# Kernel tuning notes

Measured on AMD Instinct MI355X. Metric: run time of the kernel, lower is better.

## Reference

```python
import jax, jax.numpy as jnp
import numpy as np

EMBED_DIM = 1024
NUM_HEADS = 16


def setup_inputs() -> dict:
    key = jax.random.key(0)
    k_x, k_w, k_b, k_ow, k_ob = jax.random.split(key, 5)
    B, S, E = 4, 2048, EMBED_DIM
    scale = 1.0 / np.sqrt(E)
    x = jax.random.normal(k_x, (B, S, E), dtype=jnp.float32)
    # nn.MultiheadAttention packed in-projection [3E, E] and out projection [E, E]
    in_proj_w = jax.random.uniform(k_w, (3 * E, E), dtype=jnp.float32, minval=-scale, maxval=scale)
    in_proj_b = jnp.zeros((3 * E,), dtype=jnp.float32)
    out_proj_w = jax.random.uniform(k_ow, (E, E), dtype=jnp.float32, minval=-scale, maxval=scale)
    out_proj_b = jnp.zeros((E,), dtype=jnp.float32)
    return {"x": x, "in_proj_w": in_proj_w, "in_proj_b": in_proj_b,
            "out_proj_w": out_proj_w, "out_proj_b": out_proj_b}


def reference(x, in_proj_w, in_proj_b, out_proj_w, out_proj_b):
    B, S, E = x.shape
    H = NUM_HEADS
    hd = E // H
    # packed QKV projection: [B,S,3E]
    qkv = x @ in_proj_w.T + in_proj_b
    q, k, v = jnp.split(qkv, 3, axis=-1)
    # [B,S,E] -> [B,H,S,hd]
    def to_heads(t):
        return t.reshape(B, S, H, hd).transpose(0, 2, 1, 3)
    q, k, v = to_heads(q), to_heads(k), to_heads(v)
    scale = 1.0 / jnp.sqrt(jnp.asarray(hd, dtype=x.dtype))
    scores = jnp.einsum('bhqd,bhkd->bhqk', q * scale, k)  # [B,H,S,S]
    # causal mask: position i attends to <= i (matches the -inf additive mask)
    causal = jnp.tril(jnp.ones((S, S), dtype=bool))
    scores = jnp.where(causal[None, None, :, :], scores, jnp.finfo(x.dtype).min)
    attn = jax.nn.softmax(scores, axis=-1)
    out = jnp.einsum('bhqk,bhkd->bhqd', attn, v)  # [B,H,S,hd]
    out = out.transpose(0, 2, 1, 3).reshape(B, S, E)
    return out @ out_proj_w.T + out_proj_b
```

## Files before the change

kernel.cpp:

```cpp
#include <hip/hip_runtime.h>
#include <stdint.h>

typedef _Float16 f16;
typedef _Float16 f16x2 __attribute__((ext_vector_type(2)));
typedef _Float16 f16x8 __attribute__((ext_vector_type(8)));
typedef float f32x4 __attribute__((ext_vector_type(4)));
typedef float f32x16 __attribute__((ext_vector_type(16)));
typedef uint32_t u32x4 __attribute__((ext_vector_type(4)));

#define B_   4
#define S_   2048
#define E_   1024
#define H_   16
#define HD_  64
#define BH_  (B_ * H_)

template <int N> struct IC { static constexpr int v = N; };

__device__ __forceinline__ void async_lds16(const void* g, void* l) {
    __builtin_amdgcn_global_load_lds(
        (__attribute__((address_space(1))) void*)(uintptr_t)g,
        (__attribute__((address_space(3))) void*)(uint32_t)(uintptr_t)l,
        16, 0, 0);
}

__global__ __launch_bounds__(256)
void cvt_f32_to_f16(const float* __restrict__ in, f16* __restrict__ out, int n8) {
    int i = blockIdx.x * 256 + threadIdx.x;
    if (i >= n8) return;
    const float4* p = (const float4*)in;
    float4 a = p[2 * i], b = p[2 * i + 1];
    f16x8 o;
    o[0] = (f16)a.x; o[1] = (f16)a.y; o[2] = (f16)a.z; o[3] = (f16)a.w;
    o[4] = (f16)b.x; o[5] = (f16)b.y; o[6] = (f16)b.z; o[7] = (f16)b.w;
    *(f16x8*)(out + 8 * (long)i) = o;
}

template <int MODE>
__global__ __launch_bounds__(256)
void gemm_bt(const f16* __restrict__ A, const f16* __restrict__ Bm,
             const float* __restrict__ bias, float* __restrict__ Cf,
             f16* __restrict__ qo, f16* __restrict__ ko, f16* __restrict__ vto,
             int M, int N, int K)
{
    __shared__ __align__(16) f16 As[2][128 * 32];
    __shared__ __align__(16) f16 Bs[2][128 * 32];
    const int tid = threadIdx.x;
    const int wave = tid >> 6, lane = tid & 63;
    const int lo = lane & 15, hi = lane >> 4;
    const int ntn = N >> 7;
    const int tm = blockIdx.x / ntn, tn = blockIdx.x % ntn;
    const long bm0 = (long)tm << 7, bn0 = (long)tn << 7;
    const int wr = (wave >> 1) << 6, wc = (wave & 1) << 6;

    int srow[2], sxc[2];
#pragma unroll
    for (int p = 0; p < 2; ++p) {
        const int c = p * 256 + tid;
        srow[p] = c >> 2;
        sxc[p]  = (((c & 3) ^ ((c >> 3) & 3))) * 8;
    }

#define GSTAGE(BUF, K0)  do {                                                     \
    _Pragma("unroll")                                                             \
    for (int p = 0; p < 2; ++p) {                                                 \
        const int base = (p * 256 + wave * 64) * 8;                               \
        async_lds16(A  + (bm0 + srow[p]) * K + (K0) + sxc[p], &As[BUF][base]);    \
        async_lds16(Bm + (bn0 + srow[p]) * K + (K0) + sxc[p], &Bs[BUF][base]);    \
    } } while (0)

    f32x4 acc[4][4] = {};

    auto compute = [&](auto bufc) {
        constexpr int BUF = decltype(bufc)::v;
        f16x8 af[4], bf[4];
#pragma unroll
        for (int mi = 0; mi < 4; ++mi) {
            const int row = wr + mi * 16 + lo;
            af[mi] = *(const f16x8*)&As[BUF][row * 32 + ((hi ^ ((row >> 1) & 3)) * 8)];
        }
#pragma unroll
        for (int ni = 0; ni < 4; ++ni) {
            const int row = wc + ni * 16 + lo;
            bf[ni] = *(const f16x8*)&Bs[BUF][row * 32 + ((hi ^ ((row >> 1) & 3)) * 8)];
        }
        __builtin_amdgcn_s_setprio(1);
#pragma unroll
        for (int mi = 0; mi < 4; ++mi)
#pragma unroll
            for (int ni = 0; ni < 4; ++ni)
                acc[mi][ni] = __builtin_amdgcn_mfma_f32_16x16x32_f16(
                    af[mi], bf[ni], acc[mi][ni], 0, 0, 0);
        __builtin_amdgcn_s_setprio(0);
    };

    GSTAGE(0, 0);
    __syncthreads();
    for (int k0 = 0; k0 < K; k0 += 64) {
        GSTAGE(1, k0 + 32);
        compute(IC<0>{});
        __syncthreads();
        if (k0 + 64 < K) GSTAGE(0, k0 + 64);
        compute(IC<1>{});
        __syncthreads();
    }
#undef GSTAGE

    if (MODE == 1) {
#pragma unroll
        for (int mi = 0; mi < 4; ++mi)
#pragma unroll
            for (int ni = 0; ni < 4; ++ni)
#pragma unroll
                for (int j = 0; j < 4; ++j) {
                    const long r  = bm0 + wr + mi * 16 + 4 * hi + j;
                    const int  cn = (int)bn0 + wc + ni * 16 + lo;
                    Cf[r * N + cn] = acc[mi][ni][j] + bias[cn];
                }
        return;
    }

    const int which = (int)(bn0 >> 10);
    if (which < 2) {
#pragma unroll
        for (int mi = 0; mi < 4; ++mi)
#pragma unroll
            for (int ni = 0; ni < 4; ++ni)
#pragma unroll
                for (int j = 0; j < 4; ++j) {
                    const long r  = bm0 + wr + mi * 16 + 4 * hi + j;
                    const int  cn = (int)bn0 + wc + ni * 16 + lo;
                    const int  e = cn & 1023, h = e >> 6, d = e & 63;
                    const int  b = (int)(r >> 11), s = (int)(r & 2047);
                    const long bh = (long)b * H_ + h;
                    const f16 hv = (f16)(acc[mi][ni][j] + bias[cn]);
                    if (which == 0) qo[(bh * S_ + s) * HD_ + d] = hv;
                    else            ko[(bh * S_ + s) * HD_ + d] = hv;
                }
    } else {
        f16* T = (wave < 2) ? ((f16*)As) + wave * 4096 : ((f16*)Bs) + (wave - 2) * 4096;
#pragma unroll
        for (int ni = 0; ni < 4; ++ni) {
            const int dl = ni * 16 + lo;
            const int dx = dl & 7;
#pragma unroll
            for (int mi = 0; mi < 4; ++mi)
#pragma unroll
                for (int j = 0; j < 4; ++j) {
                    const int sl = mi * 16 + 4 * hi + j;
                    const int cn = (int)bn0 + wc + ni * 16 + lo;
                    T[dl * 64 + ((((sl >> 3) ^ dx) << 3) | (sl & 7))] =
                        (f16)(acc[mi][ni][j] + bias[cn]);
                }
        }
        const int b = (int)(bm0 >> 11);
        const int sbase = (int)(bm0 & 2047) + wr;
        const int h = ((int)(bn0 & 1023) + wc) >> 6;
        const long vbase = (long)(b * H_ + h) * HD_;
#pragma unroll
        for (int it = 0; it < 8; ++it) {
            const int d = it * 8 + (lane >> 3);
            const int schunk = lane & 7;
            u32x4 val = *(const u32x4*)&T[d * 64 + ((schunk ^ (d & 7)) << 3)];
            *(u32x4*)&vto[(vbase + d) * S_ + sbase + schunk * 8] = val;
        }
    }
}

__global__ __launch_bounds__(256)
void attn_fwd(const f16* __restrict__ qb, const f16* __restrict__ kb,
              const f16* __restrict__ vtb, f16* __restrict__ ob)
{
    __shared__ __align__(16) f16 Ks[2][64 * 64];
    __shared__ __align__(16) f16 Vs[2][64 * 64];
    const int tid = threadIdx.x, wave = tid >> 6, lane = tid & 63;
    const int q32 = lane & 31, h2 = lane >> 5;
    const int bh = blockIdx.y;
    const int qtA = blockIdx.x;
    const int qtB = 15 - qtA;
    const int qwA = qtA * 128 + wave * 32;
    const int qwB = qtB * 128 + wave * 32;
    const long krow0 = (long)bh * S_;
    const long vrow0 = (long)bh * HD_;

#define STAGE(BUF, KV)  do {                                                      \
    _Pragma("unroll")                                                             \
    for (int p = 0; p < 2; ++p) {                                                 \
        const int n = p * 256 + tid;                                              \
        const int base = (p * 256 + wave * 64) * 8;                               \
        async_lds16(kb  + (krow0 + (KV) + (n & 63)) * HD_ + (n >> 6) * 8, &Ks[BUF][base]); \
        async_lds16(vtb + (vrow0 + (n & 63)) * S_ + (KV) + (n >> 6) * 8, &Vs[BUF][base]);  \
    } } while (0)

    f16x8 qfA[4], qfB[4];
    const f16 sch = (f16)0.1803368801f;
#pragma unroll
    for (int kkq = 0; kkq < 4; ++kkq) {
        qfA[kkq] = *(const f16x8*)&qb[(krow0 + qwA + q32) * HD_ + kkq * 16 + h2 * 8];
        qfB[kkq] = *(const f16x8*)&qb[(krow0 + qwB + q32) * HD_ + kkq * 16 + h2 * 8];
#pragma unroll
        for (int e = 0; e < 8; ++e) { qfA[kkq][e] *= sch; qfB[kkq][e] *= sch; }
    }

    f32x16 oaccA[2] = {}, oaccB[2] = {};
    float lA = 0.f, lB = 0.f;
    const f16x2 ones2 = { (f16)1.0f, (f16)1.0f };

    auto computeS = [&](auto bufc, auto spc, int t) {
        constexpr int BUF = decltype(bufc)::v;
        constexpr int SP  = decltype(spc)::v;
        const int qw = SP ? qwB : qwA;
        const f16x8* qf = SP ? qfB : qfA;
        f32x16* oacc = SP ? oaccB : oaccA;
        float& l_part = SP ? lB : lA;
        const int kv0 = t * 64;
        if (kv0 > qw + 31) return;
        const int qg = qw + q32;

        f32x16 sc[2] = {};
        __builtin_amdgcn_s_setprio(1);
#pragma unroll
        for (int kkq = 0; kkq < 4; ++kkq)
#pragma unroll
            for (int ni = 0; ni < 2; ++ni) {
                f16x8 kf = *(const f16x8*)&Ks[BUF][(((kkq * 2 + h2) * 64) + ni * 32 + q32) * 8];
                sc[ni] = __builtin_amdgcn_mfma_f32_32x32x16_f16(kf, qf[kkq], sc[ni], 0, 0, 0);
            }
        __builtin_amdgcn_s_setprio(0);

        const bool maskp = (kv0 + 63) > qw;
#pragma unroll
        for (int ni = 0; ni < 2; ++ni)
#pragma unroll
            for (int r = 0; r < 16; ++r) {
                float p = __builtin_amdgcn_exp2f(sc[ni][r]);
                const int kvg = kv0 + ni * 32 + (r & 3) + 8 * (r >> 2) + 4 * h2;
                if (maskp && kvg > qg) p = 0.0f;
                sc[ni][r] = p;
            }

        __builtin_amdgcn_s_setprio(1);
#pragma unroll
        for (int ni = 0; ni < 2; ++ni) {
            uint32_t u[8];
#pragma unroll
            for (int m = 0; m < 8; ++m) {
                auto hp = __builtin_amdgcn_cvt_pkrtz(sc[ni][2 * m], sc[ni][2 * m + 1]);
                u[m] = __builtin_bit_cast(uint32_t, hp);
                l_part = __builtin_amdgcn_fdot2(__builtin_bit_cast(f16x2, u[m]), ones2, l_part, false);
            }
#pragma unroll
            for (int kkv = 0; kkv < 2; ++kkv) {
                auto sA = __builtin_amdgcn_permlane32_swap(u[4 * kkv + 0], u[4 * kkv + 2], false, false);
                auto sB = __builtin_amdgcn_permlane32_swap(u[4 * kkv + 1], u[4 * kkv + 3], false, false);
                u32x4 uv = { (uint32_t)sA[0], (uint32_t)sB[0], (uint32_t)sA[1], (uint32_t)sB[1] };
                f16x8 pf = __builtin_bit_cast(f16x8, uv);
                const int kg = ni * 2 + kkv;
#pragma unroll
                for (int dh = 0; dh < 2; ++dh) {
                    f16x8 vf = *(const f16x8*)&Vs[BUF][(((kg * 2 + h2) * 64) + dh * 32 + q32) * 8];
                    oacc[dh] = __builtin_amdgcn_mfma_f32_32x32x16_f16(pf, vf, oacc[dh], 0, 0, 0);
                }
            }
        }
        __builtin_amdgcn_s_setprio(0);
    };

    const int ntB = 2 * (qtB + 1);
    STAGE(0, 0);
    __syncthreads();
    for (int t = 0; t < ntB; t += 2) {
        STAGE(1, (t + 1) * 64);
        computeS(IC<0>{}, IC<0>{}, t);
        computeS(IC<0>{}, IC<1>{}, t);
        __syncthreads();
        if (t + 2 < ntB) STAGE(0, (t + 2) * 64);
        computeS(IC<1>{}, IC<0>{}, t + 1);
        computeS(IC<1>{}, IC<1>{}, t + 1);
        __syncthreads();
    }
#undef STAGE

    const int b = bh >> 4, h = bh & 15;
    const float invA = 1.0f / (lA + __shfl_xor(lA, 32));
    const float invB = 1.0f / (lB + __shfl_xor(lB, 32));
#pragma unroll
    for (int r = 0; r < 16; ++r) {
        const int crow = (r & 3) + 8 * (r >> 2) + 4 * h2;
        const float irA = __shfl(invA, crow);
        const float irB = __shfl(invB, crow);
#pragma unroll
        for (int dh = 0; dh < 2; ++dh) {
            ob[((long)b * S_ + qwA + crow) * E_ + h * HD_ + dh * 32 + q32] = (f16)(oaccA[dh][r] * irA);
            ob[((long)b * S_ + qwB + crow) * E_ + h * HD_ + dh * 32 + q32] = (f16)(oaccB[dh][r] * irB);
        }
    }
}

extern "C" void kernel_launch(void* const* d_in, const int* in_sizes, int n_in,
                              void* d_out, int out_size, void* d_ws, size_t ws_size,
                              hipStream_t stream)
{
    (void)in_sizes; (void)n_in; (void)out_size; (void)ws_size;
    const float* x  = (const float*)d_in[0];
    const float* w1 = (const float*)d_in[1];
    const float* b1 = (const float*)d_in[2];
    const float* w2 = (const float*)d_in[3];
    const float* b2 = (const float*)d_in[4];
    float* out = (float*)d_out;

    char* ws = (char*)d_ws;
    f16* xb  = (f16*)ws;  ws += (size_t)8192 * 1024 * 2;
    f16* w1b = (f16*)ws;  ws += (size_t)3072 * 1024 * 2;
    f16* w2b = (f16*)ws;  ws += (size_t)1024 * 1024 * 2;
    f16* qb  = (f16*)ws;  ws += (size_t)BH_ * S_ * HD_ * 2;
    f16* kb  = (f16*)ws;  ws += (size_t)BH_ * S_ * HD_ * 2;
    f16* vtb = (f16*)ws;  ws += (size_t)BH_ * S_ * HD_ * 2;
    f16* ao  = (f16*)ws;  ws += (size_t)8192 * 1024 * 2;

    cvt_f32_to_f16<<<dim3(8192 * 1024 / 8 / 256), dim3(256), 0, stream>>>(x,  xb,  8192 * 1024 / 8);
    cvt_f32_to_f16<<<dim3(3072 * 1024 / 8 / 256), dim3(256), 0, stream>>>(w1, w1b, 3072 * 1024 / 8);
    cvt_f32_to_f16<<<dim3(1024 * 1024 / 8 / 256), dim3(256), 0, stream>>>(w2, w2b, 1024 * 1024 / 8);

    gemm_bt<0><<<dim3(64 * 24), dim3(256), 0, stream>>>(
        xb, w1b, b1, nullptr, qb, kb, vtb, 8192, 3072, 1024);

    attn_fwd<<<dim3(8, 64), dim3(256), 0, stream>>>(qb, kb, vtb, ao);

    gemm_bt<1><<<dim3(64 * 8), dim3(256), 0, stream>>>(
        ao, w2b, b2, out, nullptr, nullptr, nullptr, 8192, 1024, 1024);
}
```

Baseline: 170.0 us.

## Switch GEMMs to 32x32x16 MFMA and widen QKV projection tile to 256 columns

```diff
diff --git a/kernel.cpp b/kernel.cpp
--- a/kernel.cpp
+++ b/kernel.cpp
@@ -36,61 +36,69 @@
     *(f16x8*)(out + 8 * (long)i) = o;
 }
 
-template <int MODE>
+template <int MODE, int TN>
 __global__ __launch_bounds__(256)
 void gemm_bt(const f16* __restrict__ A, const f16* __restrict__ Bm,
              const float* __restrict__ bias, float* __restrict__ Cf,
              f16* __restrict__ qo, f16* __restrict__ ko, f16* __restrict__ vto,
              int M, int N, int K)
 {
+    constexpr int NF = TN >> 6;
     __shared__ __align__(16) f16 As[2][128 * 32];
-    __shared__ __align__(16) f16 Bs[2][128 * 32];
-    const int tid = threadIdx.x;
-    const int wave = tid >> 6, lane = tid & 63;
-    const int lo = lane & 15, hi = lane >> 4;
-    const int ntn = N >> 7;
+    __shared__ __align__(16) f16 Bs[2][TN * 32];
+    const int tid = threadIdx.x, wave = tid >> 6, lane = tid & 63;
+    const int q32 = lane & 31, h2 = lane >> 5;
+    const int wm = wave >> 1, wn = wave & 1;
+    const int ntn = N / TN;
     const int tm = blockIdx.x / ntn, tn = blockIdx.x % ntn;
-    const long bm0 = (long)tm << 7, bn0 = (long)tn << 7;
-    const int wr = (wave >> 1) << 6, wc = (wave & 1) << 6;
-
-    int srow[2], sxc[2];
-#pragma unroll
-    for (int p = 0; p < 2; ++p) {
-        const int c = p * 256 + tid;
-        srow[p] = c >> 2;
-        sxc[p]  = (((c & 3) ^ ((c >> 3) & 3))) * 8;
-    }
+    const long bm0 = (long)tm * 128, bn0 = (long)tn * TN;
 
 #define GSTAGE(BUF, K0)  do {                                                     \
     _Pragma("unroll")                                                             \
     for (int p = 0; p < 2; ++p) {                                                 \
-        const int base = (p * 256 + wave * 64) * 8;                               \
-        async_lds16(A  + (bm0 + srow[p]) * K + (K0) + sxc[p], &As[BUF][base]);    \
-        async_lds16(Bm + (bn0 + srow[p]) * K + (K0) + sxc[p], &Bs[BUF][base]);    \
+        const int c = p * 256 + tid;                                              \
+        const int row = c >> 2;                                                   \
+        const int sxc = ((c & 3) ^ ((c >> 3) & 3)) * 8;                           \
+        async_lds16(A + (bm0 + row) * K + (K0) + sxc,                             \
+                    &As[BUF][(p * 256 + wave * 64) * 8]);                         \
+    }                                                                             \
+    _Pragma("unroll")                                                             \
+    for (int p = 0; p < NF; ++p) {                                                \
+        const int c = p * 256 + tid;                                              \
+        const int row = c >> 2;                                                   \
+        const int sxc = ((c & 3) ^ ((c >> 3) & 3)) * 8;                           \
+        async_lds16(Bm + (bn0 + row) * K + (K0) + sxc,                            \
+                    &Bs[BUF][(p * 256 + wave * 64) * 8]);                         \
     } } while (0)
 
-    f32x4 acc[4][4] = {};
+    f32x16 acc[2][NF] = {};
 
     auto compute = [&](auto bufc) {
         constexpr int BUF = decltype(bufc)::v;
-        f16x8 af[4], bf[4];
-#pragma unroll
-        for (int mi = 0; mi < 4; ++mi) {
-            const int row = wr + mi * 16 + lo;
-            af[mi] = *(const f16x8*)&As[BUF][row * 32 + ((hi ^ ((row >> 1) & 3)) * 8)];
-        }
-#pragma unroll
-        for (int ni = 0; ni < 4; ++ni) {
-            const int row = wc + ni * 16 + lo;
-            bf[ni] = *(const f16x8*)&Bs[BUF][row * 32 + ((hi ^ ((row >> 1) & 3)) * 8)];
+        f16x8 af[2][2], bf[NF][2];
+#pragma unroll
+        for (int mi = 0; mi < 2; ++mi) {
+            const int row = wm * 64 + mi * 32 + q32;
+#pragma unroll
+            for (int kh = 0; kh < 2; ++kh)
+                af[mi][kh] = *(const f16x8*)&As[BUF][row * 32 + (((kh * 2 + h2) ^ ((row >> 1) & 3)) * 8)];
+        }
+#pragma unroll
+        for (int ni = 0; ni < NF; ++ni) {
+            const int row = wn * (TN / 2) + ni * 32 + q32;
+#pragma unroll
+            for (int kh = 0; kh < 2; ++kh)
+                bf[ni][kh] = *(const f16x8*)&Bs[BUF][row * 32 + (((kh * 2 + h2) ^ ((row >> 1) & 3)) * 8)];
         }
         __builtin_amdgcn_s_setprio(1);
 #pragma unroll
-        for (int mi = 0; mi < 4; ++mi)
-#pragma unroll
-            for (int ni = 0; ni < 4; ++ni)
-                acc[mi][ni] = __builtin_amdgcn_mfma_f32_16x16x32_f16(
-                    af[mi], bf[ni], acc[mi][ni], 0, 0, 0);
+        for (int mi = 0; mi < 2; ++mi)
+#pragma unroll
+            for (int ni = 0; ni < NF; ++ni)
+#pragma unroll
+                for (int kh = 0; kh < 2; ++kh)
+                    acc[mi][ni] = __builtin_amdgcn_mfma_f32_32x32x16_f16(
+                        af[mi][kh], bf[ni][kh], acc[mi][ni], 0, 0, 0);
         __builtin_amdgcn_s_setprio(0);
     };
 
@@ -108,14 +116,14 @@
 
     if (MODE == 1) {
 #pragma unroll
-        for (int mi = 0; mi < 4; ++mi)
-#pragma unroll
-            for (int ni = 0; ni < 4; ++ni)
-#pragma unroll
-                for (int j = 0; j < 4; ++j) {
-                    const long r  = bm0 + wr + mi * 16 + 4 * hi + j;
-                    const int  cn = (int)bn0 + wc + ni * 16 + lo;
-                    Cf[r * N + cn] = acc[mi][ni][j] + bias[cn];
+        for (int mi = 0; mi < 2; ++mi)
+#pragma unroll
+            for (int ni = 0; ni < NF; ++ni)
+#pragma unroll
+                for (int reg = 0; reg < 16; ++reg) {
+                    const long r = bm0 + wm * 64 + mi * 32 + (reg & 3) + 8 * (reg >> 2) + 4 * h2;
+                    const int cn = (int)bn0 + wn * (TN / 2) + ni * 32 + q32;
+                    Cf[r * N + cn] = acc[mi][ni][reg] + bias[cn];
                 }
         return;
     }
@@ -123,46 +131,51 @@
     const int which = (int)(bn0 >> 10);
     if (which < 2) {
 #pragma unroll
-        for (int mi = 0; mi < 4; ++mi)
-#pragma unroll
-            for (int ni = 0; ni < 4; ++ni)
-#pragma unroll
-                for (int j = 0; j < 4; ++j) {
-                    const long r  = bm0 + wr + mi * 16 + 4 * hi + j;
-                    const int  cn = (int)bn0 + wc + ni * 16 + lo;
-                    const int  e = cn & 1023, h = e >> 6, d = e & 63;
-                    const int  b = (int)(r >> 11), s = (int)(r & 2047);
+        for (int mi = 0; mi < 2; ++mi)
+#pragma unroll
+            for (int ni = 0; ni < NF; ++ni)
+#pragma unroll
+                for (int reg = 0; reg < 16; ++reg) {
+                    const long r = bm0 + wm * 64 + mi * 32 + (reg & 3) + 8 * (reg >> 2) + 4 * h2;
+                    const int cn = (int)bn0 + wn * (TN / 2) + ni * 32 + q32;
+                    const int e = cn & 1023, h = e >> 6, d = e & 63;
+                    const int b = (int)(r >> 11), s = (int)(r & 2047);
                     const long bh = (long)b * H_ + h;
-                    const f16 hv = (f16)(acc[mi][ni][j] + bias[cn]);
+                    const f16 hv = (f16)(acc[mi][ni][reg] + bias[cn]);
                     if (which == 0) qo[(bh * S_ + s) * HD_ + d] = hv;
                     else            ko[(bh * S_ + s) * HD_ + d] = hv;
                 }
     } else {
-        f16* T = (wave < 2) ? ((f16*)As) + wave * 4096 : ((f16*)Bs) + (wave - 2) * 4096;
-#pragma unroll
-        for (int ni = 0; ni < 4; ++ni) {
-            const int dl = ni * 16 + lo;
-            const int dx = dl & 7;
-#pragma unroll
-            for (int mi = 0; mi < 4; ++mi)
-#pragma unroll
-                for (int j = 0; j < 4; ++j) {
-                    const int sl = mi * 16 + 4 * hi + j;
-                    const int cn = (int)bn0 + wc + ni * 16 + lo;
-                    T[dl * 64 + ((((sl >> 3) ^ dx) << 3) | (sl & 7))] =
-                        (f16)(acc[mi][ni][j] + bias[cn]);
-                }
-        }
-        const int b = (int)(bm0 >> 11);
-        const int sbase = (int)(bm0 & 2047) + wr;
-        const int h = ((int)(bn0 & 1023) + wc) >> 6;
-        const long vbase = (long)(b * H_ + h) * HD_;
-#pragma unroll
-        for (int it = 0; it < 8; ++it) {
-            const int d = it * 8 + (lane >> 3);
-            const int schunk = lane & 7;
-            u32x4 val = *(const u32x4*)&T[d * 64 + ((schunk ^ (d & 7)) << 3)];
-            *(u32x4*)&vto[(vbase + d) * S_ + sbase + schunk * 8] = val;
+        f16* T = ((f16*)Bs) + wave * 4096;
+#pragma unroll
+        for (int half = 0; half < 2; ++half) {
+#pragma unroll
+            for (int nn = 0; nn < 2; ++nn) {
+                const int ni = half * 2 + nn;
+                const int dl = nn * 32 + q32;
+                const int dx = dl & 7;
+                const int cn = (int)bn0 + wn * 128 + ni * 32 + q32;
+#pragma unroll
+                for (int mi = 0; mi < 2; ++mi)
+#pragma unroll
+                    for (int reg = 0; reg < 16; ++reg) {
+                        const int sl = mi * 32 + (reg & 3) + 8 * (reg >> 2) + 4 * h2;
+                        T[dl * 64 + ((((sl >> 3) ^ dx) << 3) | (sl & 7))] =
+                            (f16)(acc[mi][ni][reg] + bias[cn]);
+                    }
+            }
+            const int b = (int)(bm0 >> 11);
+            const int sbase = (int)(bm0 & 2047) + wm * 64;
+            const int col0 = (int)(bn0 & 1023) + wn * 128 + half * 64;
+            const int h = col0 >> 6;
+            const long vbase = (long)(b * H_ + h) * HD_;
+#pragma unroll
+            for (int it = 0; it < 8; ++it) {
+                const int d = it * 8 + (lane >> 3);
+                const int schunk = lane & 7;
+                u32x4 val = *(const u32x4*)&T[d * 64 + ((schunk ^ (d & 7)) << 3)];
+                *(u32x4*)&vto[(vbase + d) * S_ + sbase + schunk * 8] = val;
+            }
         }
     }
 }
@@ -322,11 +335,11 @@
     cvt_f32_to_f16<<<dim3(3072 * 1024 / 8 / 256), dim3(256), 0, stream>>>(w1, w1b, 3072 * 1024 / 8);
     cvt_f32_to_f16<<<dim3(1024 * 1024 / 8 / 256), dim3(256), 0, stream>>>(w2, w2b, 1024 * 1024 / 8);
 
-    gemm_bt<0><<<dim3(64 * 24), dim3(256), 0, stream>>>(
+    gemm_bt<0, 256><<<dim3(64 * 12), dim3(256), 0, stream>>>(
         xb, w1b, b1, nullptr, qb, kb, vtb, 8192, 3072, 1024);
 
     attn_fwd<<<dim3(8, 64), dim3(256), 0, stream>>>(qb, kb, vtb, ao);
 
-    gemm_bt<1><<<dim3(64 * 8), dim3(256), 0, stream>>>(
+    gemm_bt<1, 128><<<dim3(64 * 8), dim3(256), 0, stream>>>(
         ao, w2b, b2, out, nullptr, nullptr, nullptr, 8192, 1024, 1024);
 }
```

After: 178.9 us. 1.05x slower.

## Add dedicated QKV GEMM with 128x256 tiles and triple-buffered async pipeline

Applied to the files above, without the earlier changes.

```diff
diff --git a/kernel.cpp b/kernel.cpp
--- a/kernel.cpp
+++ b/kernel.cpp
@@ -34,6 +34,134 @@
     o[0] = (f16)a.x; o[1] = (f16)a.y; o[2] = (f16)a.z; o[3] = (f16)a.w;
     o[4] = (f16)b.x; o[5] = (f16)b.y; o[6] = (f16)b.z; o[7] = (f16)b.w;
     *(f16x8*)(out + 8 * (long)i) = o;
+}
+
+__global__ __launch_bounds__(512)
+void gemm_qkv(const f16* __restrict__ A, const f16* __restrict__ Bm,
+              const float* __restrict__ bias,
+              f16* __restrict__ qo, f16* __restrict__ ko, f16* __restrict__ vto)
+{
+    constexpr int K = 1024, N = 3072, NT = 16;
+    __shared__ __align__(16) f16 L[3][(128 + 256) * 64];
+    const int tid = threadIdx.x, wave = tid >> 6, lane = tid & 63;
+    const int lo = lane & 15, hi = lane >> 4;
+    const int bid0 = blockIdx.x;
+    const int bid = (bid0 & 7) * 96 + (bid0 >> 3);
+    const int tm = bid / 12, tn = bid % 12;
+    const long bm0 = (long)tm * 128, bn0 = (long)tn * 256;
+    const int wr = (wave >> 2) * 64, wc = (wave & 3) * 64;
+
+#define STAGE6(BUF, T)  do {                                                      \
+    const long kk = (long)(T) * 64;                                               \
+    _Pragma("unroll")                                                             \
+    for (int j = 0; j < 2; ++j) {                                                 \
+        const int c = j * 512 + tid;                                              \
+        const int row = c >> 3, ch = c & 7;                                       \
+        async_lds16(A + (bm0 + row) * K + kk + ((ch ^ (row & 7)) * 8),            \
+                    &L[BUF][(j * 512 + wave * 64) * 8]);                          \
+    }                                                                             \
+    _Pragma("unroll")                                                             \
+    for (int j = 0; j < 4; ++j) {                                                 \
+        const int c = j * 512 + tid;                                              \
+        const int row = c >> 3, ch = c & 7;                                       \
+        async_lds16(Bm + (bn0 + row) * K + kk + ((ch ^ (row & 7)) * 8),           \
+                    &L[BUF][8192 + (j * 512 + wave * 64) * 8]);                   \
+    } } while (0)
+
+    f32x4 acc[4][4] = {};
+
+    auto tile = [&](auto bufc, int t) {
+        constexpr int BUF = decltype(bufc)::v;
+        constexpr int SBUF = (BUF + 2) % 3;
+        if (t + 2 < NT) STAGE6(SBUF, t + 2);
+        f16x8 af[2][4], bf[2][4];
+#pragma unroll
+        for (int kh = 0; kh < 2; ++kh) {
+#pragma unroll
+            for (int mi = 0; mi < 4; ++mi) {
+                const int r = wr + mi * 16 + lo;
+                af[kh][mi] = *(const f16x8*)&L[BUF][(r * 8 + ((kh * 4 + hi) ^ (r & 7))) * 8];
+            }
+#pragma unroll
+            for (int ni = 0; ni < 4; ++ni) {
+                const int r = wc + ni * 16 + lo;
+                bf[kh][ni] = *(const f16x8*)&L[BUF][8192 + (r * 8 + ((kh * 4 + hi) ^ (r & 7))) * 8];
+            }
+        }
+        __builtin_amdgcn_s_setprio(1);
+#pragma unroll
+        for (int kh = 0; kh < 2; ++kh)
+#pragma unroll
+            for (int mi = 0; mi < 4; ++mi)
+#pragma unroll
+                for (int ni = 0; ni < 4; ++ni)
+                    acc[mi][ni] = __builtin_amdgcn_mfma_f32_16x16x32_f16(
+                        af[kh][mi], bf[kh][ni], acc[mi][ni], 0, 0, 0);
+        __builtin_amdgcn_s_setprio(0);
+        if (t + 2 < NT) asm volatile("s_waitcnt vmcnt(6)" ::: "memory");
+        else            asm volatile("s_waitcnt vmcnt(0)" ::: "memory");
+        __builtin_amdgcn_sched_barrier(0);
+        __builtin_amdgcn_s_barrier();
+    };
+
+    STAGE6(0, 0);
+    STAGE6(1, 1);
+    asm volatile("s_waitcnt vmcnt(6)" ::: "memory");
+    __builtin_amdgcn_sched_barrier(0);
+    __builtin_amdgcn_s_barrier();
+    for (int t = 0; t < 15; t += 3) {
+        tile(IC<0>{}, t);
+        tile(IC<1>{}, t + 1);
+        tile(IC<2>{}, t + 2);
+    }
+    tile(IC<0>{}, 15);
+#undef STAGE6
+
+    const int which = (int)(bn0 >> 10);
+    if (which < 2) {
+#pragma unroll
+        for (int mi = 0; mi < 4; ++mi)
+#pragma unroll
+            for (int ni = 0; ni < 4; ++ni)
+#pragma unroll
+                for (int j = 0; j < 4; ++j) {
+                    const long r  = bm0 + wr + mi * 16 + 4 * hi + j;
+                    const int  cn = (int)bn0 + wc + ni * 16 + lo;
+                    const int  e = cn & 1023, h = e >> 6, d = e & 63;
+                    const int  b = (int)(r >> 11), s = (int)(r & 2047);
+                    const long bh = (long)b * H_ + h;
+                    const f16 hv = (f16)(acc[mi][ni][j] + bias[cn]);
+                    if (which == 0) qo[(bh * S_ + s) * HD_ + d] = hv;
+                    else            ko[(bh * S_ + s) * HD_ + d] = hv;
+                }
+    } else {
+        f16* T = ((f16*)L) + wave * 4096;
+#pragma unroll
+        for (int ni = 0; ni < 4; ++ni) {
+            const int dl = ni * 16 + lo;
+            const int dx = dl & 7;
+#pragma unroll
+            for (int mi = 0; mi < 4; ++mi)
+#pragma unroll
+                for (int j = 0; j < 4; ++j) {
+                    const int sl = mi * 16 + 4 * hi + j;
+                    const int cn = (int)bn0 + wc + ni * 16 + lo;
+                    T[dl * 64 + ((((sl >> 3) ^ dx) << 3) | (sl & 7))] =
+                        (f16)(acc[mi][ni][j] + bias[cn]);
+                }
+        }
+        const int b = (int)(bm0 >> 11);
+        const int sbase = (int)(bm0 & 2047) + wr;
+        const int h = ((int)(bn0 & 1023) + wc) >> 6;
+        const long vbase = (long)(b * H_ + h) * HD_;
+#pragma unroll
+        for (int it = 0; it < 8; ++it) {
+            const int d = it * 8 + (lane >> 3);
+            const int schunk = lane & 7;
+            u32x4 val = *(const u32x4*)&T[d * 64 + ((schunk ^ (d & 7)) << 3)];
+            *(u32x4*)&vto[(vbase + d) * S_ + sbase + schunk * 8] = val;
+        }
+    }
 }
 
 template <int MODE>
@@ -119,52 +247,7 @@
                 }
         return;
     }
-
-    const int which = (int)(bn0 >> 10);
-    if (which < 2) {
-#pragma unroll
-        for (int mi = 0; mi < 4; ++mi)
-#pragma unroll
-            for (int ni = 0; ni < 4; ++ni)
-#pragma unroll
-                for (int j = 0; j < 4; ++j) {
-                    const long r  = bm0 + wr + mi * 16 + 4 * hi + j;
-                    const int  cn = (int)bn0 + wc + ni * 16 + lo;
-                    const int  e = cn & 1023, h = e >> 6, d = e & 63;
-                    const int  b = (int)(r >> 11), s = (int)(r & 2047);
-                    const long bh = (long)b * H_ + h;
-                    const f16 hv = (f16)(acc[mi][ni][j] + bias[cn]);
-                    if (which == 0) qo[(bh * S_ + s) * HD_ + d] = hv;
-                    else            ko[(bh * S_ + s) * HD_ + d] = hv;
-                }
-    } else {
-        f16* T = (wave < 2) ? ((f16*)As) + wave * 4096 : ((f16*)Bs) + (wave - 2) * 4096;
-#pragma unroll
-        for (int ni = 0; ni < 4; ++ni) {
-            const int dl = ni * 16 + lo;
-            const int dx = dl & 7;
-#pragma unroll
-            for (int mi = 0; mi < 4; ++mi)
-#pragma unroll
-                for (int j = 0; j < 4; ++j) {
-                    const int sl = mi * 16 + 4 * hi + j;
-                    const int cn = (int)bn0 + wc + ni * 16 + lo;
-                    T[dl * 64 + ((((sl >> 3) ^ dx) << 3) | (sl & 7))] =
-                        (f16)(acc[mi][ni][j] + bias[cn]);
-                }
-        }
-        const int b = (int)(bm0 >> 11);
-        const int sbase = (int)(bm0 & 2047) + wr;
-        const int h = ((int)(bn0 & 1023) + wc) >> 6;
-        const long vbase = (long)(b * H_ + h) * HD_;
-#pragma unroll
-        for (int it = 0; it < 8; ++it) {
-            const int d = it * 8 + (lane >> 3);
-            const int schunk = lane & 7;
-            u32x4 val = *(const u32x4*)&T[d * 64 + ((schunk ^ (d & 7)) << 3)];
-            *(u32x4*)&vto[(vbase + d) * S_ + sbase + schunk * 8] = val;
-        }
-    }
+    (void)qo; (void)ko; (void)vto;
 }
 
 __global__ __launch_bounds__(256)
@@ -322,8 +405,7 @@
     cvt_f32_to_f16<<<dim3(3072 * 1024 / 8 / 256), dim3(256), 0, stream>>>(w1, w1b, 3072 * 1024 / 8);
     cvt_f32_to_f16<<<dim3(1024 * 1024 / 8 / 256), dim3(256), 0, stream>>>(w2, w2b, 1024 * 1024 / 8);
 
-    gemm_bt<0><<<dim3(64 * 24), dim3(256), 0, stream>>>(
-        xb, w1b, b1, nullptr, qb, kb, vtb, 8192, 3072, 1024);
+    gemm_qkv<<<dim3(768), dim3(512), 0, stream>>>(xb, w1b, b1, qb, kb, vtb);
 
     attn_fwd<<<dim3(8, 64), dim3(256), 0, stream>>>(qb, kb, vtb, ao);
 
```

After: 159.2 us. 1.07x faster.
